# Optimization experiments

Measured on AMD Instinct MI355X. Metric: run time of the kernel, lower is better.

The kernel has to match this reference:

```python
import jax, jax.numpy as jnp
import numpy as np

B, L, D, H = 4, 1024, 768, 12
DH = D // H  # 64


def setup_inputs() -> dict:
    key = jax.random.key(0)
    kx, kk, kq, kv = jax.random.split(key, 4)
    # Original uses torch.rand (uniform [0,1)); scale by 1/D so pre-softmax
    # logits stay in a numerically sane range (same math, better conditioning).
    scale = 1.0 / D
    x = jax.random.normal(kx, (B, L, D), dtype=jnp.float32)
    k = jax.random.uniform(kk, (H, D, D), dtype=jnp.float32) * scale
    q = jax.random.uniform(kq, (H, D, D), dtype=jnp.float32) * scale
    v = jax.random.uniform(kv, (H, DH, D), dtype=jnp.float32) * scale
    return {"x": x, "k": k, "q": q, "v": v}


def reference(x, k, q, v):
    # x: [B, L, D]; torch permutes to [B, D, L] then 'bdl,ncd->bncl';
    # equivalent directly: 'bld,ncd->bncl'.
    K = jnp.einsum('bld,ncd->bncl', x, k)   # [B, H, D, L]
    Q = jnp.einsum('bld,ncd->bncl', x, q)   # [B, H, D, L]
    V = jnp.einsum('bld,ncd->bncl', x, v)   # [B, H, DH, L]
    scores = jnp.einsum('bndl,bndm->bnlm', Q, K)        # [B, H, L, L]
    S = jax.nn.softmax(scores, axis=-1)                  # softmax over dim 3
    R = jnp.einsum('bnkl,bndl->bndk', S, V)              # [B, H, DH, L]
    R = R.reshape(x.shape[0], D, -1)                     # [B, D, L]
    return jnp.transpose(R, (0, 2, 1))                   # [B, L, D]
```

## Files before the change

### kernel.cpp

```cpp
#include <hip/hip_runtime.h>
#include <hip/hip_bf16.h>
#include <stdint.h>
#include <stddef.h>

typedef unsigned short u16;
typedef __attribute__((ext_vector_type(8))) short short8;
typedef __attribute__((ext_vector_type(4))) float f32x4;
typedef __attribute__((ext_vector_type(16))) float f32x16;

#define NB 4
#define NL 1024
#define ND 768
#define NH 12
#define NDH 64

__device__ __forceinline__ u16 f2bf(float f) {
  __hip_bfloat16 h = __float2bfloat16(f);
  return *reinterpret_cast<u16*>(&h);
}
__device__ __forceinline__ float bf2f(u16 u) {
  __hip_bfloat16 h;
  *reinterpret_cast<u16*>(&h) = u;
  return __bfloat162float(h);
}

__device__ __forceinline__ void load16_to_lds(const u16* g, u16* l) {
  __builtin_amdgcn_global_load_lds(
      (__attribute__((address_space(1))) void*)(uintptr_t)g,
      (__attribute__((address_space(3))) void*)(uint32_t)(uintptr_t)l,
      16, 0, 0);
}

__global__ __launch_bounds__(256) void prep_inputs_kernel(
    const float* __restrict__ qI, const float* __restrict__ kI,
    u16* __restrict__ qT, u16* __restrict__ kTp,
    const float* __restrict__ x, u16* __restrict__ xb, int n4A,
    const float* __restrict__ vI, u16* __restrict__ vb, int n4B) {
  __shared__ float tile[32][33];
  int hz = blockIdx.z;
  if (hz == 2 * NH) {
    int i = (blockIdx.x + 24 * blockIdx.y) * 256 + threadIdx.x;
    int stride = 576 * 256;
    int tot = n4A + n4B;
    for (; i < tot; i += stride) {
      const float4* src;
      ushort4* dst;
      int j;
      if (i < n4A) { src = (const float4*)x; dst = (ushort4*)xb; j = i; }
      else         { src = (const float4*)vI; dst = (ushort4*)vb; j = i - n4A; }
      float4 f = src[j];
      ushort4 o;
      o.x = f2bf(f.x); o.y = f2bf(f.y); o.z = f2bf(f.z); o.w = f2bf(f.w);
      dst[j] = o;
    }
    return;
  }
  int h = (hz < NH) ? hz : hz - NH;
  const float* src = ((hz < NH) ? qI : kI) + (size_t)h * ND * ND;
  u16* dst = ((hz < NH) ? qT : kTp) + (size_t)h * ND * ND;
  int c0 = blockIdx.x * 32, r0 = blockIdx.y * 32;
  int tx = threadIdx.x & 31, ty = threadIdx.x >> 5;
#pragma unroll
  for (int i = 0; i < 32; i += 8)
    tile[ty + i][tx] = src[(size_t)(r0 + ty + i) * ND + c0 + tx];
  __syncthreads();
  int p = tx & 15, j = (tx >> 4) * 8 + ty;
#pragma unroll
  for (int i = 0; i < 32; i += 16) {
    ushort2 o;
    o.x = f2bf(tile[2 * p][j + i]);
    o.y = f2bf(tile[2 * p + 1][j + i]);
    *(ushort2*)&dst[(size_t)(c0 + j + i) * ND + r0 + 2 * p] = o;
  }
}

template <bool BF16_OUT, int IM, int IN, int KDIM, int LDC>
__global__ __launch_bounds__(256, 4) void gemm_bt(
    const u16* __restrict__ A, const u16* __restrict__ Bm, void* __restrict__ Cv,
    long sAb, long sAn, long sAz,
    long sBb, long sBn, long sBz,
    long sCb, long sCn, long sCz,
    int p0) {
  constexpr int BK = 64;
  constexpr int MTILE = IM * 64;
  constexpr int NTILE = IN * 64;
  constexpr int CPR = BK / 8;
  constexpr int ACH = MTILE * CPR / 256;
  constexpr int BCH = NTILE * CPR / 256;
  __shared__ __align__(16) u16 As[MTILE * BK];
  __shared__ __align__(16) u16 Bs[NTILE * BK];

  int id = blockIdx.x + gridDim.x * (blockIdx.y + gridDim.y * blockIdx.z);
  int total = gridDim.x * gridDim.y * gridDim.z;
  int xx, yy, zz;
  if ((total & 7) == 0) {
    int per = total >> 3;
    int wk = (id & 7) * per + (id >> 3);
    xx = wk % gridDim.x;
    int g2 = wk / gridDim.x;
    yy = g2 % gridDim.y;
    zz = g2 / gridDim.y;
  } else {
    xx = blockIdx.x; yy = blockIdx.y; zz = blockIdx.z;
  }

  int g = p0 + zz;
  int b = g / NH, n = g % NH;
  A  += (size_t)b * sAb + (size_t)n * sAn + (size_t)zz * sAz;
  Bm += (size_t)b * sBb + (size_t)n * sBn + (size_t)zz * sBz;
  size_t cOff = (size_t)b * sCb + (size_t)n * sCn + (size_t)zz * sCz;

  int m0 = yy * MTILE, n0 = xx * NTILE;
  int t = threadIdx.x;
  int lane = t & 63, w = t >> 6;
  int m32 = lane & 31, kg = lane >> 5;
  int wm = w >> 1, wn = w & 1;

  const u16* gAb;
  const u16* gBb;
  {
    int r = t / CPR;
    int cc = (t & (CPR - 1)) ^ (r & 7);
    gAb = A + (size_t)(m0 + r) * KDIM + cc * 8;
    gBb = Bm + (size_t)(n0 + r) * KDIM + cc * 8;
  }

  f32x16 acc[IM][IN];
#pragma unroll
  for (int i = 0; i < IM; i++)
#pragma unroll
    for (int j = 0; j < IN; j++)
#pragma unroll
      for (int r = 0; r < 16; r++) acc[i][j][r] = 0.f;

#pragma unroll 1
  for (int k0 = 0; k0 < KDIM; k0 += BK) {
    __syncthreads();
#pragma unroll
    for (int u = 0; u < ACH; u++)
      load16_to_lds(gAb + (size_t)u * 32 * KDIM, &As[(size_t)(u * 256 + w * 64) * 8]);
    gAb += BK;
#pragma unroll
    for (int u = 0; u < BCH; u++)
      load16_to_lds(gBb + (size_t)u * 32 * KDIM, &Bs[(size_t)(u * 256 + w * 64) * 8]);
    gBb += BK;
    __syncthreads();

#pragma unroll
    for (int kc = 0; kc < 2; kc++) {
      short8 af[IM][2], bfr[IN][2];
#pragma unroll
      for (int i = 0; i < IM; i++) {
        int row = wm * (IM * 32) + i * 32 + m32;
#pragma unroll
        for (int h = 0; h < 2; h++) {
          int ck = (kc * 4 + h * 2 + kg) ^ (row & 7);
          af[i][h] = *(const short8*)&As[row * BK + ck * 8];
        }
      }
#pragma unroll
      for (int j = 0; j < IN; j++) {
        int row = wn * (IN * 32) + j * 32 + m32;
#pragma unroll
        for (int h = 0; h < 2; h++) {
          int ck = (kc * 4 + h * 2 + kg) ^ (row & 7);
          bfr[j][h] = *(const short8*)&Bs[row * BK + ck * 8];
        }
      }
#pragma unroll
      for (int i = 0; i < IM; i++)
#pragma unroll
        for (int j = 0; j < IN; j++) {
          acc[i][j] = __builtin_amdgcn_mfma_f32_32x32x16_bf16(af[i][0], bfr[j][0], acc[i][j], 0, 0, 0);
          acc[i][j] = __builtin_amdgcn_mfma_f32_32x32x16_bf16(af[i][1], bfr[j][1], acc[i][j], 0, 0, 0);
        }
    }
  }

#pragma unroll
  for (int i = 0; i < IM; i++) {
#pragma unroll
    for (int j = 0; j < IN; j++) {
      int colg = n0 + wn * (IN * 32) + j * 32 + m32;
#pragma unroll
      for (int r = 0; r < 16; r++) {
        int rowg = m0 + wm * (IM * 32) + i * 32 + (r & 3) + 8 * (r >> 2) + 4 * kg;
        float vv = acc[i][j][r];
        if (BF16_OUT) {
          ((u16*)Cv)[cOff + (size_t)rowg * LDC + colg] = f2bf(vv);
        } else {
          ((float*)Cv)[cOff + (size_t)rowg * LDC + colg] = vv;
        }
      }
    }
  }
}

__global__ __launch_bounds__(256, 4) void gemm_prep(
    const u16* __restrict__ kT, const u16* __restrict__ qT, u16* __restrict__ MTp,
    const u16* __restrict__ vb, const u16* __restrict__ xb, u16* __restrict__ V2p) {
  constexpr int BK = 64;
  constexpr int KDIM = ND;
  constexpr int CPR = BK / 8;
  constexpr long DD = (long)ND * ND;
  constexpr long LD = (long)NL * ND;
  __shared__ __align__(16) u16 As[128 * BK];
  __shared__ __align__(16) u16 Bs[128 * BK];

  int id = blockIdx.x + gridDim.x * (blockIdx.y + gridDim.y * blockIdx.z);
  int total = gridDim.x * gridDim.y * gridDim.z;
  int per = total >> 3;
  int wk = (id & 7) * per + (id >> 3);
  int xx = wk % gridDim.x;
  int g2 = wk / gridDim.x;
  int yy = g2 % gridDim.y;
  int zz = g2 / gridDim.y;

  const u16* A;
  const u16* Bm;
  u16* C;
  int ldc;
  if (zz < NH) {
    if (xx >= 6) return;
    A = kT + (size_t)zz * DD;
    Bm = qT + (size_t)zz * DD;
    C = MTp + (size_t)zz * DD;
    ldc = ND;
  } else {
    int b = zz - NH;
    A = vb;
    Bm = xb + (size_t)b * LD;
    C = V2p + (size_t)b * NH * NDH * NL;
    ldc = NL;
  }

  int m0 = yy * 128, n0 = xx * 128;
  int t = threadIdx.x;
  int lane = t & 63, w = t >> 6;
  int m32 = lane & 31, kg = lane >> 5;
  int wm = w >> 1, wn = w & 1;

  const u16* gAb;
  const u16* gBb;
  {
    int r = t / CPR;
    int cc = (t & (CPR - 1)) ^ (r & 7);
    gAb = A + (size_t)(m0 + r) * KDIM + cc * 8;
    gBb = Bm + (size_t)(n0 + r) * KDIM + cc * 8;
  }

  f32x16 acc[2][2];
#pragma unroll
  for (int i = 0; i < 2; i++)
#pragma unroll
    for (int j = 0; j < 2; j++)
#pragma unroll
      for (int r = 0; r < 16; r++) acc[i][j][r] = 0.f;

#pragma unroll 1
  for (int k0 = 0; k0 < KDIM; k0 += BK) {
    __syncthreads();
#pragma unroll
    for (int u = 0; u < 4; u++)
      load16_to_lds(gAb + (size_t)u * 32 * KDIM, &As[(size_t)(u * 256 + w * 64) * 8]);
    gAb += BK;
#pragma unroll
    for (int u = 0; u < 4; u++)
      load16_to_lds(gBb + (size_t)u * 32 * KDIM, &Bs[(size_t)(u * 256 + w * 64) * 8]);
    gBb += BK;
    __syncthreads();

#pragma unroll
    for (int kc = 0; kc < 2; kc++) {
      short8 af[2][2], bfr[2][2];
#pragma unroll
      for (int i = 0; i < 2; i++) {
        int row = wm * 64 + i * 32 + m32;
#pragma unroll
        for (int h = 0; h < 2; h++) {
          int ck = (kc * 4 + h * 2 + kg) ^ (row & 7);
          af[i][h] = *(const short8*)&As[row * BK + ck * 8];
        }
      }
#pragma unroll
      for (int j = 0; j < 2; j++) {
        int row = wn * 64 + j * 32 + m32;
#pragma unroll
        for (int h = 0; h < 2; h++) {
          int ck = (kc * 4 + h * 2 + kg) ^ (row & 7);
          bfr[j][h] = *(const short8*)&Bs[row * BK + ck * 8];
        }
      }
#pragma unroll
      for (int i = 0; i < 2; i++)
#pragma unroll
        for (int j = 0; j < 2; j++) {
          acc[i][j] = __builtin_amdgcn_mfma_f32_32x32x16_bf16(af[i][0], bfr[j][0], acc[i][j], 0, 0, 0);
          acc[i][j] = __builtin_amdgcn_mfma_f32_32x32x16_bf16(af[i][1], bfr[j][1], acc[i][j], 0, 0, 0);
        }
    }
  }

#pragma unroll
  for (int i = 0; i < 2; i++) {
#pragma unroll
    for (int j = 0; j < 2; j++) {
      int colg = n0 + wn * 64 + j * 32 + m32;
#pragma unroll
      for (int r = 0; r < 16; r++) {
        int rowg = m0 + wm * 64 + i * 32 + (r & 3) + 8 * (r >> 2) + 4 * kg;
        C[(size_t)rowg * ldc + colg] = f2bf(acc[i][j][r]);
      }
    }
  }
}

template <int OUTMODE, int KDIM, int LDC>
__global__ __launch_bounds__(512, 2) void gemm256_8p(
    const u16* __restrict__ A, const u16* __restrict__ Bm, void* __restrict__ Cv,
    long sAb, long sAn, long sAz,
    long sBb, long sBn, long sBz,
    long sCb, long sCn, long sCz,
    int p0) {
  constexpr int BK = 64;
  constexpr int NT = KDIM / BK;
  constexpr int NC = NT / 2;
  static_assert(KDIM % 128 == 0 && NC >= 2, "need even #K-tiles and >=2 cycles");
  __shared__ __align__(16) u16 As[2][256 * BK];
  __shared__ __align__(16) u16 Bs[2][256 * BK];

  int id = blockIdx.x + gridDim.x * (blockIdx.y + gridDim.y * blockIdx.z);
  int total = gridDim.x * gridDim.y * gridDim.z;
  int xx, yy, zz;
  if ((total & 7) == 0) {
    int per = total >> 3;
    int wk = (id & 7) * per + (id >> 3);
    xx = wk % gridDim.x;
    int g2 = wk / gridDim.x;
    yy = g2 % gridDim.y;
    zz = g2 / gridDim.y;
  } else {
    xx = blockIdx.x; yy = blockIdx.y; zz = blockIdx.z;
  }

  int g = p0 + zz;
  int b = g / NH, n = g % NH;
  A  += (size_t)b * sAb + (size_t)n * sAn + (size_t)zz * sAz;
  Bm += (size_t)b * sBb + (size_t)n * sBn + (size_t)zz * sBz;
  size_t cOff = (size_t)b * sCb + (size_t)n * sCn + (size_t)zz * sCz;

  int m0 = yy * 256, n0 = xx * 256;
  int t = threadIdx.x;
  int lane = t & 63, w = t >> 6;
  int wm = w >> 2, wn = w & 3;
  int l15 = lane & 15, q4 = lane >> 4;

  int r0 = t >> 3;
  int cc0 = (t & 7) ^ (r0 & 7);
  const u16* gA = A + (size_t)(m0 + r0) * KDIM + cc0 * 8;
  const u16* gB = Bm + (size_t)(n0 + r0) * KDIM + cc0 * 8;
  int wslab = w * 512;

#define STG_A1(d, h, u, kt) load16_to_lds( \
    gA + (size_t)((h) * 128 + (u) * 64) * KDIM + (size_t)(kt) * BK, \
    &As[d][((h) * 128 + (u) * 64) * BK + wslab])
#define STG_B1(d, h, u, kt) load16_to_lds( \
    gB + (size_t)((h) * 128 + (u) * 64) * KDIM + (size_t)(kt) * BK, \
    &Bs[d][((h) * 128 + (u) * 64) * BK + wslab])
#define STG_A2(d, h, kt) do { STG_A1(d, h, 0, kt); STG_A1(d, h, 1, kt); } while (0)
#define STG_B2(d, h, kt) do { STG_B1(d, h, 0, kt); STG_B1(d, h, 1, kt); } while (0)

#define READ_A(d, qm, dst) do { \
  _Pragma("unroll") for (int fm = 0; fm < 4; fm++) { \
    int row = (qm) * 128 + wm * 64 + fm * 16 + l15; \
    _Pragma("unroll") for (int ks = 0; ks < 2; ks++) { \
      int ck = (ks * 4 + q4) ^ (row & 7); \
      dst[fm][ks] = *(const short8*)&As[d][row * BK + ck * 8]; \
    } \
  } \
} while (0)

#define READ_B(d, qn, dst) do { \
  _Pragma("unroll") for (int fn = 0; fn < 2; fn++) { \
    int row = (qn) * 128 + wn * 32 + fn * 16 + l15; \
    _Pragma("unroll") for (int ks = 0; ks < 2; ks++) { \
      int ck = (ks * 4 + q4) ^ (row & 7); \
      dst[fn][ks] = *(const short8*)&Bs[d][row * BK + ck * 8]; \
    } \
  } \
} while (0)

#define MF_Q(qm, qn, AR, BR) do { \
  __builtin_amdgcn_s_setprio(1); \
  _Pragma("unroll") for (int ks = 0; ks < 2; ks++) \
    _Pragma("unroll") for (int fm = 0; fm < 4; fm++) \
      _Pragma("unroll") for (int fn = 0; fn < 2; fn++) \
        acc[qm][qn][fm][fn] = __builtin_amdgcn_mfma_f32_16x16x32_bf16( \
            AR[fm][ks], BR[fn][ks], acc[qm][qn][fm][fn], 0, 0, 0); \
  __builtin_amdgcn_s_setprio(0); \
} while (0)

#define PH_SYNC() do { \
  __builtin_amdgcn_s_barrier(); \
  asm volatile("s_waitcnt lgkmcnt(0)" ::: "memory"); \
  __builtin_amdgcn_sched_barrier(0); \
} while (0)
#define PH_END() do { \
  __builtin_amdgcn_s_barrier(); \
  __builtin_amdgcn_sched_barrier(0); \
} while (0)

  f32x4 acc[2][2][4][2];
#pragma unroll
  for (int qm = 0; qm < 2; qm++)
#pragma unroll
    for (int qn = 0; qn < 2; qn++)
#pragma unroll
      for (int fm = 0; fm < 4; fm++)
#pragma unroll
        for (int fn = 0; fn < 2; fn++)
          acc[qm][qn][fm][fn] = (f32x4){0.f, 0.f, 0.f, 0.f};

  STG_A2(0, 0, 0); STG_A2(0, 1, 0);
  STG_B2(0, 0, 0); STG_B2(0, 1, 0);
  STG_A2(1, 0, 1); STG_A2(1, 1, 1);
  STG_B2(1, 0, 1); STG_B2(1, 1, 1);
  asm volatile("s_waitcnt vmcnt(8)" ::: "memory");
  __builtin_amdgcn_s_barrier();
  __builtin_amdgcn_sched_barrier(0);

#pragma unroll 1
  for (int cyc = 0; cyc < NC; ++cyc) {
    int t0 = cyc * 2;
    bool full = (cyc + 1 < NC);
    short8 af0[4][2], af1[4][2], bq0[2][2], bq1[2][2];

    READ_A(0, 0, af0); READ_B(0, 0, bq0);
    PH_SYNC(); MF_Q(0, 0, af0, bq0); PH_END();
    READ_B(0, 1, bq1);
    if (full) { STG_A2(0, 0, t0 + 2); STG_B2(0, 0, t0 + 2); }
    PH_SYNC(); MF_Q(0, 1, af0, bq1); PH_END();
    READ_A(0, 1, af1);
    if (full) STG_B2(0, 1, t0 + 2);
    PH_SYNC(); MF_Q(1, 0, af1, bq0); PH_END();
    if (full) STG_A2(0, 1, t0 + 2);
    __builtin_amdgcn_s_barrier();
    MF_Q(1, 1, af1, bq1);
    __builtin_amdgcn_sched_barrier(0);
    if (full) asm volatile("s_waitcnt vmcnt(8)" ::: "memory");
    else      asm volatile("s_waitcnt vmcnt(0)" ::: "memory");
    PH_END();

    READ_A(1, 0, af0); READ_B(1, 0, bq0);
    PH_SYNC(); MF_Q(0, 0, af0, bq0); PH_END();
    READ_B(1, 1, bq1);
    if (full) { STG_A2(1, 0, t0 + 3); STG_B2(1, 0, t0 + 3); }
    PH_SYNC(); MF_Q(0, 1, af0, bq1); PH_END();
    READ_A(1, 1, af1);
    if (full) STG_B2(1, 1, t0 + 3);
    PH_SYNC(); MF_Q(1, 0, af1, bq0); PH_END();
    if (full) {
      STG_A2(1, 1, t0 + 3);
      __builtin_amdgcn_s_barrier();
      MF_Q(1, 1, af1, bq1);
      __builtin_amdgcn_sched_barrier(0);
      asm volatile("s_waitcnt vmcnt(8)" ::: "memory");
      PH_END();
    } else {
      __builtin_amdgcn_s_barrier();
      MF_Q(1, 1, af1, bq1);
    }
  }

#pragma unroll
  for (int qm = 0; qm < 2; qm++)
#pragma unroll
    for (int qn = 0; qn < 2; qn++)
#pragma unroll
      for (int fm = 0; fm < 4; fm++)
#pragma unroll
        for (int fn = 0; fn < 2; fn++) {
          int colg = n0 + qn * 128 + wn * 32 + fn * 16 + l15;
#pragma unroll
          for (int r = 0; r < 4; r++) {
            int rowg = m0 + qm * 128 + wm * 64 + fm * 16 + q4 * 4 + r;
            float vv = acc[qm][qn][fm][fn][r];
            if (OUTMODE == 2) vv = __expf(vv);
            if (OUTMODE >= 1) {
              ((u16*)Cv)[cOff + (size_t)rowg * LDC + colg] = f2bf(vv);
            } else {
              ((float*)Cv)[cOff + (size_t)rowg * LDC + colg] = vv;
            }
          }
        }
#undef STG_A1
#undef STG_B1
#undef STG_A2
#undef STG_B2
#undef READ_A
#undef READ_B
#undef MF_Q
#undef PH_SYNC
#undef PH_END
}

__global__ __launch_bounds__(256) void softmax_pv_kernel(
    const u16* __restrict__ Sb, const u16* __restrict__ V2, float* __restrict__ out,
    int p0) {
  __shared__ __align__(16) u16 Ps[64 * 128];
  __shared__ __align__(16) u16 Vs[64 * 128];

  int id = blockIdx.x + gridDim.x * blockIdx.y;
  int total = gridDim.x * gridDim.y;
  int xx, zz;
  if ((total & 7) == 0) {
    int per = total >> 3;
    int wk = (id & 7) * per + (id >> 3);
    xx = wk & 15; zz = wk >> 4;
  } else {
    xx = blockIdx.x; zz = blockIdx.y;
  }

  int g = p0 + zz;
  int b = g / NH, n = g % NH;
  const u16* S = Sb + (size_t)zz * NL * NL;
  const u16* V = V2 + (size_t)g * NDH * NL;

  int l0 = xx * 64;
  int t = threadIdx.x;
  int lane = t & 63, w = t >> 6;
  int row16 = lane & 15, q = lane >> 4;
  int rs = row16 & 7;

  f32x4 acc[5];
#pragma unroll
  for (int j = 0; j < 5; j++) acc[j] = (f32x4){0.f, 0.f, 0.f, 0.f};

  short8 onesf;
  {
    short val = (row16 == 0) ? (short)0x3F80 : (short)0;
#pragma unroll
    for (int e = 0; e < 8; e++) onesf[e] = val;
  }

  const u16* ssrc[4];
  const u16* vsrc[4];
#pragma unroll
  for (int u = 0; u < 4; u++) {
    int c = u * 256 + t;
    int r = c >> 4, cc = (c & 15) ^ (r & 7);
    ssrc[u] = S + (size_t)(l0 + r) * NL + cc * 8;
    vsrc[u] = V + (size_t)r * NL + cc * 8;
  }

#pragma unroll 1
  for (int mt = 0; mt < 8; mt++) {
    int mo = mt * 128;
    __syncthreads();
#pragma unroll
    for (int u = 0; u < 4; u++)
      load16_to_lds(ssrc[u] + mo, &Ps[(size_t)(u * 256 + w * 64) * 8]);
#pragma unroll
    for (int u = 0; u < 4; u++)
      load16_to_lds(vsrc[u] + mo, &Vs[(size_t)(u * 256 + w * 64) * 8]);
    __syncthreads();

#pragma unroll
    for (int kk = 0; kk < 4; kk++) {
      int ch = ((kk * 4 + q) ^ rs) * 16;
      int lrow = w * 16 + row16;
      short8 raw = *(const short8*)((const char*)Ps + lrow * 256 + ch);
      short8 af;
#pragma unroll
      for (int e = 0; e < 8; e++) af[e] = (short)f2bf(__expf(bf2f((u16)raw[e])));
      short8 bfr[4];
#pragma unroll
      for (int j = 0; j < 4; j++) {
        int dh = j * 16 + row16;
        bfr[j] = *(const short8*)((const char*)Vs + dh * 256 + ch);
      }
#pragma unroll
      for (int j = 0; j < 4; j++)
        acc[j] = __builtin_amdgcn_mfma_f32_16x16x32_bf16(af, bfr[j], acc[j], 0, 0, 0);
      acc[4] = __builtin_amdgcn_mfma_f32_16x16x32_bf16(af, onesf, acc[4], 0, 0, 0);
    }
  }

#pragma unroll
  for (int r = 0; r < 4; r++) {
    float sum = __shfl(acc[4][r], lane & 48, 64);
    float inv = 1.0f / sum;
    int row = l0 + w * 16 + q * 4 + r;
    float* op = out + ((size_t)b * NL + row) * ND + n * NDH;
#pragma unroll
    for (int j = 0; j < 4; j++)
      op[j * 16 + row16] = acc[j][r] * inv;
  }
}

extern "C" void kernel_launch(void* const* d_in, const int* in_sizes, int n_in,
                              void* d_out, int out_size, void* d_ws, size_t ws_size,
                              hipStream_t stream) {
  (void)in_sizes; (void)n_in; (void)out_size;
  const float* x  = (const float*)d_in[0];
  const float* kI = (const float*)d_in[1];
  const float* qI = (const float*)d_in[2];
  const float* vI = (const float*)d_in[3];
  float* out = (float*)d_out;

  size_t off = 0;
  char* wsb = (char*)d_ws;
  auto alloc = [&](size_t bytes) -> char* {
    char* p = wsb + off;
    off += (bytes + 255) & ~(size_t)255;
    return p;
  };
  u16* xb = (u16*)alloc((size_t)NB * NL * ND * 2);
  u16* vb = (u16*)alloc((size_t)NH * NDH * ND * 2);
  u16* MT = (u16*)alloc((size_t)NH * ND * ND * 2);
  u16* V2 = (u16*)alloc((size_t)NB * NH * NDH * NL * 2);
  size_t fixedSz = off;

  u16* qT = (u16*)alloc((size_t)NH * ND * ND * 2);
  u16* kT = (u16*)alloc((size_t)NH * ND * ND * 2);
  size_t scratchEndQK = off;

  const size_t Tsz  = (size_t)NL * ND * 2;
  const size_t Ssz  = (size_t)NL * NL * 2;
  const size_t perPair = Tsz + Ssz;

  int chunk = NB * NH;
  {
    size_t avail = ws_size > fixedSz ? ws_size - fixedSz : 0;
    size_t maxChunk = avail / perPair;
    if (maxChunk < 1) maxChunk = 1;
    if (maxChunk < (size_t)chunk) {
      int passes = (int)(((size_t)NB * NH + maxChunk - 1) / maxChunk);
      chunk = (NB * NH + passes - 1) / passes;
    }
  }
  off = fixedSz;
  u16* T  = (u16*)alloc((size_t)chunk * Tsz);
  u16* Sb = (u16*)alloc((size_t)chunk * Ssz);
  if (off < scratchEndQK) off = scratchEndQK;

  const long DD  = (long)ND * ND;
  const long LD  = (long)NL * ND;
  const long LL  = (long)NL * NL;

  {
    int n4A = NB * NL * ND / 4;
    int n4B = NH * NDH * ND / 4;
    prep_inputs_kernel<<<dim3(24, 24, 2 * NH + 1), dim3(256), 0, stream>>>(
        qI, kI, qT, kT, x, xb, n4A, vI, vb, n4B);
  }

  gemm_prep<<<dim3(8, 6, 16), dim3(256), 0, stream>>>(kT, qT, MT, vb, xb, V2);

  for (int p0 = 0; p0 < NB * NH; p0 += chunk) {
    int c = NB * NH - p0;
    if (c > chunk) c = chunk;
    gemm_bt<true, 2, 2, 768, ND><<<dim3(6, 8, c), dim3(256), 0, stream>>>(
        xb, MT, T,
        LD, 0, 0,  0, DD, 0,  0, 0, LD, p0);
    gemm256_8p<1, 768, NL><<<dim3(4, 4, c), dim3(512), 0, stream>>>(
        T, xb, Sb,
        0, 0, LD,  LD, 0, 0,  0, 0, LL, p0);
    softmax_pv_kernel<<<dim3(16, c), dim3(256), 0, stream>>>(Sb, V2, out, p0);
  }
}
```

Measured before the change: 300.2 us.

## Make 256x256 score GEMM persistent and prefetch next tile during epilogue

Turns the score GEMM into a persistent kernel launched with 256 blocks, where each block walks tiles with a stride of 256. While the last K-cycle of the current tile runs, the block stages the first two K-tiles of its next tile into LDS, so the prologue load overlaps compute and the epilogue. This targets launch and tail overhead and the pipeline refill cost between tiles. It adds per-tile address resolution and more register pressure, and it relies on the grid size of 256 matching the CU count for good balance.

New measurement: 295.2 us. About the same (-1.6%).

```diff
diff --git a/kernel.cpp b/kernel.cpp
--- a/kernel.cpp
+++ b/kernel.cpp
@@ -316,12 +316,12 @@
 }
 
 template <int OUTMODE, int KDIM, int LDC>
-__global__ __launch_bounds__(512, 2) void gemm256_8p(
-    const u16* __restrict__ A, const u16* __restrict__ Bm, void* __restrict__ Cv,
+__global__ __launch_bounds__(512, 2) void gemm256_pers(
+    const u16* __restrict__ A0, const u16* __restrict__ B0, void* __restrict__ Cv,
     long sAb, long sAn, long sAz,
     long sBb, long sBn, long sBz,
     long sCb, long sCn, long sCz,
-    int p0) {
+    int p0, int tX, int tY, int nTiles) {
   constexpr int BK = 64;
   constexpr int NT = KDIM / BK;
   constexpr int NC = NT / 2;
@@ -329,46 +329,49 @@
   __shared__ __align__(16) u16 As[2][256 * BK];
   __shared__ __align__(16) u16 Bs[2][256 * BK];
 
-  int id = blockIdx.x + gridDim.x * (blockIdx.y + gridDim.y * blockIdx.z);
-  int total = gridDim.x * gridDim.y * gridDim.z;
-  int xx, yy, zz;
-  if ((total & 7) == 0) {
-    int per = total >> 3;
-    int wk = (id & 7) * per + (id >> 3);
-    xx = wk % gridDim.x;
-    int g2 = wk / gridDim.x;
-    yy = g2 % gridDim.y;
-    zz = g2 / gridDim.y;
-  } else {
-    xx = blockIdx.x; yy = blockIdx.y; zz = blockIdx.z;
-  }
-
-  int g = p0 + zz;
-  int b = g / NH, n = g % NH;
-  A  += (size_t)b * sAb + (size_t)n * sAn + (size_t)zz * sAz;
-  Bm += (size_t)b * sBb + (size_t)n * sBn + (size_t)zz * sBz;
-  size_t cOff = (size_t)b * sCb + (size_t)n * sCn + (size_t)zz * sCz;
-
-  int m0 = yy * 256, n0 = xx * 256;
+  int beta = blockIdx.x;
+  if (beta >= nTiles) return;
+
   int t = threadIdx.x;
   int lane = t & 63, w = t >> 6;
   int wm = w >> 2, wn = w & 3;
   int l15 = lane & 15, q4 = lane >> 4;
-
   int r0 = t >> 3;
   int cc0 = (t & 7) ^ (r0 & 7);
-  const u16* gA = A + (size_t)(m0 + r0) * KDIM + cc0 * 8;
-  const u16* gB = Bm + (size_t)(n0 + r0) * KDIM + cc0 * 8;
   int wslab = w * 512;
 
-#define STG_A1(d, h, u, kt) load16_to_lds( \
-    gA + (size_t)((h) * 128 + (u) * 64) * KDIM + (size_t)(kt) * BK, \
+  struct TileP { const u16* pA; const u16* pB; size_t co; int m0, n0; };
+  auto resolve = [&](int tau, TileP& tp) {
+    int wk;
+    if ((nTiles & 7) == 0) {
+      int per = nTiles >> 3;
+      wk = (tau & 7) * per + (tau >> 3);
+    } else {
+      wk = tau;
+    }
+    int xx = wk % tX;
+    int g2 = wk / tX;
+    int yy = g2 % tY;
+    int zz = g2 / tY;
+    int g = p0 + zz;
+    int b = g / NH, n = g % NH;
+    tp.m0 = yy * 256;
+    tp.n0 = xx * 256;
+    tp.pA = A0 + (size_t)b * sAb + (size_t)n * sAn + (size_t)zz * sAz +
+            (size_t)(tp.m0 + r0) * KDIM + cc0 * 8;
+    tp.pB = B0 + (size_t)b * sBb + (size_t)n * sBn + (size_t)zz * sBz +
+            (size_t)(tp.n0 + r0) * KDIM + cc0 * 8;
+    tp.co = (size_t)b * sCb + (size_t)n * sCn + (size_t)zz * sCz;
+  };
+
+#define STG_A1(P, d, h, u, kt) load16_to_lds( \
+    (P) + (size_t)((h) * 128 + (u) * 64) * KDIM + (size_t)(kt) * BK, \
     &As[d][((h) * 128 + (u) * 64) * BK + wslab])
-#define STG_B1(d, h, u, kt) load16_to_lds( \
-    gB + (size_t)((h) * 128 + (u) * 64) * KDIM + (size_t)(kt) * BK, \
+#define STG_B1(P, d, h, u, kt) load16_to_lds( \
+    (P) + (size_t)((h) * 128 + (u) * 64) * KDIM + (size_t)(kt) * BK, \
     &Bs[d][((h) * 128 + (u) * 64) * BK + wslab])
-#define STG_A2(d, h, kt) do { STG_A1(d, h, 0, kt); STG_A1(d, h, 1, kt); } while (0)
-#define STG_B2(d, h, kt) do { STG_B1(d, h, 0, kt); STG_B1(d, h, 1, kt); } while (0)
+#define STG_A2(P, d, h, kt) do { STG_A1(P, d, h, 0, kt); STG_A1(P, d, h, 1, kt); } while (0)
+#define STG_B2(P, d, h, kt) do { STG_B1(P, d, h, 0, kt); STG_B1(P, d, h, 1, kt); } while (0)
 
 #define READ_A(d, qm, dst) do { \
   _Pragma("unroll") for (int fm = 0; fm < 4; fm++) { \
@@ -421,78 +424,106 @@
         for (int fn = 0; fn < 2; fn++)
           acc[qm][qn][fm][fn] = (f32x4){0.f, 0.f, 0.f, 0.f};
 
-  STG_A2(0, 0, 0); STG_A2(0, 1, 0);
-  STG_B2(0, 0, 0); STG_B2(0, 1, 0);
-  STG_A2(1, 0, 1); STG_A2(1, 1, 1);
-  STG_B2(1, 0, 1); STG_B2(1, 1, 1);
+  int tau = beta;
+  TileP cur, nxt;
+  resolve(tau, cur);
+  bool hasNext = (tau + 256) < nTiles;
+  if (hasNext) resolve(tau + 256, nxt);
+
+  STG_A2(cur.pA, 0, 0, 0); STG_A2(cur.pA, 0, 1, 0);
+  STG_B2(cur.pB, 0, 0, 0); STG_B2(cur.pB, 0, 1, 0);
+  STG_A2(cur.pA, 1, 0, 1); STG_A2(cur.pA, 1, 1, 1);
+  STG_B2(cur.pB, 1, 0, 1); STG_B2(cur.pB, 1, 1, 1);
   asm volatile("s_waitcnt vmcnt(8)" ::: "memory");
   __builtin_amdgcn_s_barrier();
   __builtin_amdgcn_sched_barrier(0);
 
+  while (true) {
 #pragma unroll 1
-  for (int cyc = 0; cyc < NC; ++cyc) {
-    int t0 = cyc * 2;
-    bool full = (cyc + 1 < NC);
-    short8 af0[4][2], af1[4][2], bq0[2][2], bq1[2][2];
-
-    READ_A(0, 0, af0); READ_B(0, 0, bq0);
-    PH_SYNC(); MF_Q(0, 0, af0, bq0); PH_END();
-    READ_B(0, 1, bq1);
-    if (full) { STG_A2(0, 0, t0 + 2); STG_B2(0, 0, t0 + 2); }
-    PH_SYNC(); MF_Q(0, 1, af0, bq1); PH_END();
-    READ_A(0, 1, af1);
-    if (full) STG_B2(0, 1, t0 + 2);
-    PH_SYNC(); MF_Q(1, 0, af1, bq0); PH_END();
-    if (full) STG_A2(0, 1, t0 + 2);
-    __builtin_amdgcn_s_barrier();
-    MF_Q(1, 1, af1, bq1);
-    __builtin_amdgcn_sched_barrier(0);
-    if (full) asm volatile("s_waitcnt vmcnt(8)" ::: "memory");
-    else      asm volatile("s_waitcnt vmcnt(0)" ::: "memory");
-    PH_END();
-
-    READ_A(1, 0, af0); READ_B(1, 0, bq0);
-    PH_SYNC(); MF_Q(0, 0, af0, bq0); PH_END();
-    READ_B(1, 1, bq1);
-    if (full) { STG_A2(1, 0, t0 + 3); STG_B2(1, 0, t0 + 3); }
-    PH_SYNC(); MF_Q(0, 1, af0, bq1); PH_END();
-    READ_A(1, 1, af1);
-    if (full) STG_B2(1, 1, t0 + 3);
-    PH_SYNC(); MF_Q(1, 0, af1, bq0); PH_END();
-    if (full) {
-      STG_A2(1, 1, t0 + 3);
+    for (int cyc = 0; cyc < NC; ++cyc) {
+      int t0 = cyc * 2;
+      bool inTile = (t0 + 2 < NT);
+      bool doStg = inTile || hasNext;
+      const u16* sA2 = inTile ? cur.pA : nxt.pA;
+      const u16* sB2 = inTile ? cur.pB : nxt.pB;
+      int k2 = inTile ? (t0 + 2) : 0;
+      int k3 = inTile ? (t0 + 3) : 1;
+      short8 af0[4][2], af1[4][2], bq0[2][2], bq1[2][2];
+
+      READ_A(0, 0, af0); READ_B(0, 0, bq0);
+      PH_SYNC(); MF_Q(0, 0, af0, bq0); PH_END();
+      READ_B(0, 1, bq1);
+      if (doStg) { STG_A2(sA2, 0, 0, k2); STG_B2(sB2, 0, 0, k2); }
+      PH_SYNC(); MF_Q(0, 1, af0, bq1); PH_END();
+      READ_A(0, 1, af1);
+      if (doStg) STG_B2(sB2, 0, 1, k2);
+      PH_SYNC(); MF_Q(1, 0, af1, bq0); PH_END();
+      if (doStg) STG_A2(sA2, 0, 1, k2);
       __builtin_amdgcn_s_barrier();
       MF_Q(1, 1, af1, bq1);
       __builtin_amdgcn_sched_barrier(0);
-      asm volatile("s_waitcnt vmcnt(8)" ::: "memory");
+      if (doStg) asm volatile("s_waitcnt vmcnt(8)" ::: "memory");
+      else       asm volatile("s_waitcnt vmcnt(0)" ::: "memory");
       PH_END();
-    } else {
-      __builtin_amdgcn_s_barrier();
-      MF_Q(1, 1, af1, bq1);
-    }
-  }
-
-#pragma unroll
-  for (int qm = 0; qm < 2; qm++)
-#pragma unroll
-    for (int qn = 0; qn < 2; qn++)
-#pragma unroll
-      for (int fm = 0; fm < 4; fm++)
-#pragma unroll
-        for (int fn = 0; fn < 2; fn++) {
-          int colg = n0 + qn * 128 + wn * 32 + fn * 16 + l15;
-#pragma unroll
-          for (int r = 0; r < 4; r++) {
-            int rowg = m0 + qm * 128 + wm * 64 + fm * 16 + q4 * 4 + r;
-            float vv = acc[qm][qn][fm][fn][r];
-            if (OUTMODE == 2) vv = __expf(vv);
-            if (OUTMODE >= 1) {
-              ((u16*)Cv)[cOff + (size_t)rowg * LDC + colg] = f2bf(vv);
-            } else {
-              ((float*)Cv)[cOff + (size_t)rowg * LDC + colg] = vv;
+
+      READ_A(1, 0, af0); READ_B(1, 0, bq0);
+      PH_SYNC(); MF_Q(0, 0, af0, bq0); PH_END();
+      READ_B(1, 1, bq1);
+      if (doStg) { STG_A2(sA2, 1, 0, k3); STG_B2(sB2, 1, 0, k3); }
+      PH_SYNC(); MF_Q(0, 1, af0, bq1); PH_END();
+      READ_A(1, 1, af1);
+      if (doStg) STG_B2(sB2, 1, 1, k3);
+      PH_SYNC(); MF_Q(1, 0, af1, bq0); PH_END();
+      if (doStg) {
+        STG_A2(sA2, 1, 1, k3);
+        __builtin_amdgcn_s_barrier();
+        MF_Q(1, 1, af1, bq1);
+        __builtin_amdgcn_sched_barrier(0);
+        asm volatile("s_waitcnt vmcnt(8)" ::: "memory");
+        PH_END();
+      } else {
+        __builtin_amdgcn_s_barrier();
+        MF_Q(1, 1, af1, bq1);
+      }
+    }
+
+#pragma unroll
+    for (int qm = 0; qm < 2; qm++)
+#pragma unroll
+      for (int qn = 0; qn < 2; qn++)
+#pragma unroll
+        for (int fm = 0; fm < 4; fm++)
+#pragma unroll
+          for (int fn = 0; fn < 2; fn++) {
+            int colg = cur.n0 + qn * 128 + wn * 32 + fn * 16 + l15;
+#pragma unroll
+            for (int r = 0; r < 4; r++) {
+              int rowg = cur.m0 + qm * 128 + wm * 64 + fm * 16 + q4 * 4 + r;
+              float vv = acc[qm][qn][fm][fn][r];
+              if (OUTMODE == 2) vv = __expf(vv);
+              if (OUTMODE >= 1) {
+                ((u16*)Cv)[cur.co + (size_t)rowg * LDC + colg] = f2bf(vv);
+              } else {
+                ((float*)Cv)[cur.co + (size_t)rowg * LDC + colg] = vv;
+              }
             }
           }
-        }
+
+    if (!hasNext) break;
+    tau += 256;
+    cur = nxt;
+    hasNext = (tau + 256) < nTiles;
+    if (hasNext) resolve(tau + 256, nxt);
+#pragma unroll
+    for (int qm = 0; qm < 2; qm++)
+#pragma unroll
+      for (int qn = 0; qn < 2; qn++)
+#pragma unroll
+        for (int fm = 0; fm < 4; fm++)
+#pragma unroll
+          for (int fn = 0; fn < 2; fn++)
+            acc[qm][qn][fm][fn] = (f32x4){0.f, 0.f, 0.f, 0.f};
+  }
 #undef STG_A1
 #undef STG_B1
 #undef STG_A2
@@ -663,9 +694,9 @@
     gemm_bt<true, 2, 2, 768, ND><<<dim3(6, 8, c), dim3(256), 0, stream>>>(
         xb, MT, T,
         LD, 0, 0,  0, DD, 0,  0, 0, LD, p0);
-    gemm256_8p<1, 768, NL><<<dim3(4, 4, c), dim3(512), 0, stream>>>(
+    gemm256_pers<1, 768, NL><<<dim3(256), dim3(512), 0, stream>>>(
         T, xb, Sb,
-        0, 0, LD,  LD, 0, 0,  0, 0, LL, p0);
+        0, 0, LD,  LD, 0, 0,  0, 0, LL, p0, 4, 4, 16 * c);
     softmax_pv_kernel<<<dim3(16, c), dim3(256), 0, stream>>>(Sb, V2, out, p0);
   }
 }
```
